# Performance work log

Hardware: AMD Instinct MI355X
Metric: run time of the kernel (lower is better)

## Reference

```python
import jax, jax.numpy as jnp
import numpy as np

# Fixed hierarchical grouping of the 15 regions into 5 groups of 3 (from split_regions)
SPLIT_IDX = np.array([[0, 1, 8], [2, 4, 6], [3, 5, 7], [9, 11, 13], [10, 12, 14]])
BN_EPS = 1e-5


def _bn_relu(x, g, b):
    # BatchNorm over (batch, spatial) dims in training-stats mode, then ReLU
    mu = jnp.mean(x, axis=(0, 2, 3), keepdims=True)
    var = jnp.var(x, axis=(0, 2, 3), keepdims=True)
    xn = (x - mu) * jax.lax.rsqrt(var + BN_EPS)
    return jax.nn.relu(xn * g[None, :, None, None] + b[None, :, None, None])


def _local_agg(x, params):
    # x: [B, Cin, G, K]; pointwise conv (1x1) -> BN -> ReLU per layer, then max over K
    for W, g, b in params:
        x = jnp.einsum('oi,bigk->bogk', W, x)
        x = _bn_relu(x, g, b)
    return jnp.max(x, axis=-1)  # [B, Cout, G]


def setup_inputs() -> dict:
    key = jax.random.key(0)
    ks = jax.random.split(key, 8)
    B, G, K = 32, 15, 2048
    inp = {"local_regions": jax.random.normal(ks[0], (B, G, K, 3), jnp.float32)}
    chans = [(3, 64, 64), (67, 128, 128), (131, 256, 256)]
    ki = 1
    for li, (c0, c1, c2) in enumerate(chans):
        for wi, (co, ci) in enumerate([(c1, c0), (c2, c1)]):
            inp[f"la{li}_w{wi}"] = jax.random.normal(ks[ki], (co, ci), jnp.float32) * (1.0 / np.sqrt(ci))
            inp[f"la{li}_g{wi}"] = jnp.ones((co,), jnp.float32)
            inp[f"la{li}_b{wi}"] = jnp.zeros((co,), jnp.float32)
            ki += 1
    return inp


def reference(local_regions,
              la0_w0, la0_g0, la0_b0, la0_w1, la0_g1, la0_b1,
              la1_w0, la1_g0, la1_b0, la1_w1, la1_g1, la1_b1,
              la2_w0, la2_g0, la2_b0, la2_w1, la2_g1, la2_b1):
    la0 = [(la0_w0, la0_g0, la0_b0), (la0_w1, la0_g1, la0_b1)]
    la1 = [(la1_w0, la1_g0, la1_b0), (la1_w1, la1_g1, la1_b1)]
    la2 = [(la2_w0, la2_g0, la2_b0), (la2_w1, la2_g1, la2_b1)]
    idx = jnp.asarray(SPLIT_IDX)

    x = jnp.transpose(local_regions, (0, 3, 1, 2))  # [B, 3, 15, K]
    centroids_1 = jnp.mean(x, axis=-1)              # [B, 3, 15]
    relative_1 = x - centroids_1[..., None]
    lf1 = _local_agg(relative_1, la0)               # [B, 64, 15]
    local_features = jnp.concatenate([centroids_1, lf1], axis=1)  # [B, 67, 15]

    # level 2: regroup 15 regions into [5, 3]
    lf1_s = jnp.transpose(lf1, (0, 2, 1))[:, idx, :]         # [B, 5, 3, 64]
    lr2 = jnp.transpose(centroids_1, (0, 2, 1))[:, idx, :]   # [B, 5, 3, 3]
    c2 = jnp.mean(lr2, axis=2)                               # [B, 5, 3]
    rel2 = lr2 - c2[:, :, None, :]
    feats2 = jnp.concatenate([rel2, lf1_s], axis=-1)         # [B, 5, 3, 67]
    feats2 = jnp.transpose(feats2, (0, 3, 1, 2))             # [B, 67, 5, 3]
    lf2 = _local_agg(feats2, la1)                            # [B, 128, 5]

    # level 3: global
    c3 = jnp.mean(c2, axis=1)                                # [B, 3]
    rel3 = c2 - c3[:, None, :]                               # [B, 5, 3]
    lf2 = jnp.concatenate([jnp.transpose(rel3, (0, 2, 1)), lf2], axis=1)  # [B, 131, 5]
    lf2 = lf2[:, :, None, :]                                 # [B, 131, 1, 5]
    gf = _local_agg(lf2, la2)                                # [B, 256, 1]
    return gf.squeeze(2), local_features
```

## Files before the change

### kernel.cpp

```cpp
#include <hip/hip_runtime.h>
#include <math.h>

#define BB 32
#define GG 15
#define KK 2048
#define NB 480
#define N1F 983040.0f
#define EPS 1e-5f
#define PZN ((int)0xAAAAAAAA)

typedef _Float16 half8 __attribute__((ext_vector_type(8)));
typedef float f32x4 __attribute__((ext_vector_type(4)));

#define WS_CENT  0
#define WS_MN    1920
#define GSREL    63360
#define GBN1     63600
#define G2A      67440
#define G2B      67952
#define G3A      68464
#define G3B      69488
#define FSREL    70512
#define FBN1     70520
#define F2A      70648
#define F2B      70904
#define F3A      71160
#define F3B      71672
#define CNT_GRP  72184
#define CNT_SUP  72376
#define CNT_DONE 72382

#define SMEMF 7936

__device__ const int SIDX[15] = {0,1,8, 2,4,6, 3,5,7, 9,11,13, 10,12,14};

__device__ __forceinline__ float wave_sum(float v){
    for (int off = 32; off; off >>= 1) v += __shfl_down(v, off, 64);
    return v;
}
__device__ __forceinline__ float aloadf(const float* p){
    return __hip_atomic_load(p, __ATOMIC_RELAXED, __HIP_MEMORY_SCOPE_AGENT);
}
__device__ __forceinline__ int aloadi(const int* p){
    return __hip_atomic_load(p, __ATOMIC_RELAXED, __HIP_MEMORY_SCOPE_AGENT);
}
template<int SLP, class Fold>
__device__ __forceinline__ void gbar(int* wsi, int idx, int gi, int ngrp,
                                     int* sflag, Fold fold){
    __syncthreads();
    if (threadIdx.x == 0)
        sflag[0] = (atomicAdd(&wsi[CNT_GRP + idx*32 + gi], 1) == PZN + 15) ? 1 : 0;
    __syncthreads();
    if (sflag[0]) {
        if (threadIdx.x == 0)
            sflag[1] = (atomicAdd(&wsi[CNT_SUP + idx], 1) == PZN + ngrp - 1) ? 1 : 0;
        __syncthreads();
        if (sflag[1]) {
            fold();
            __syncthreads();
            if (threadIdx.x == 0) atomicExch(&wsi[CNT_DONE + idx], 1);
        }
    }
    if (threadIdx.x == 0) {
        int g = 0;
        while (aloadi(&wsi[CNT_DONE + idx]) != 1 && ++g < 4000000)
            __builtin_amdgcn_s_sleep(SLP);
    }
    __syncthreads();
    asm volatile("" ::: "memory");
}

__global__ void __launch_bounds__(256, 2) mega(
        const float* __restrict__ x,
        const float* __restrict__ w00, const float* __restrict__ g00, const float* __restrict__ b00,
        const float* __restrict__ w01, const float* __restrict__ g01, const float* __restrict__ b01,
        const float* __restrict__ w10, const float* __restrict__ g10, const float* __restrict__ b10,
        const float* __restrict__ w11, const float* __restrict__ g11, const float* __restrict__ b11,
        const float* __restrict__ w20, const float* __restrict__ g20, const float* __restrict__ b20,
        const float* __restrict__ w21, const float* __restrict__ g21, const float* __restrict__ b21,
        float* __restrict__ ws, float* __restrict__ out) {
    __shared__ __align__(16) float smemf[SMEMF];
    float* xls  = smemf;
    float* redM = smemf + 6144; float* redN = smemf + 6400;
    float* redS = smemf + 6656; float* redQ = smemf + 6912;
    float* bcast= smemf + 7168;
    int*   sflag= (int*)(smemf + 7916);
    float* s1ls  = smemf;
    float* t1ls  = smemf + 64;
    float* centls= smemf + 128;
    float* c2ls  = smemf + 176;
    float* c3ls  = smemf + 192;
    float* f2ls  = smemf + 256;
    float* vls   = smemf + 1280;
    float* f3ls  = smemf + 3200;
    float* u3ls  = smemf + 3968;
    int* wsi = (int*)ws;

    int bid = blockIdx.x, tid = threadIdx.x;
    int b_ = bid / GG, g_ = bid % GG;
    int wv = tid >> 6, lane = tid & 63, l15 = lane & 15, quad = lane >> 4;
    int gi = bid >> 4;

    {
        const float4* xp4 = (const float4*)(x + (size_t)bid * KK * 3);
        float4* xls4 = (float4*)xls;
        #pragma unroll
        for (int i = 0; i < 6; i++) xls4[i*256 + tid] = xp4[i*256 + tid];
        __syncthreads();
        float m[9] = {0,0,0,0,0,0,0,0,0};
        float a[24];
        const float* bp = &xls[tid*24];
        #pragma unroll
        for (int i = 0; i < 6; i++)
            *reinterpret_cast<float4*>(&a[i*4]) = *reinterpret_cast<const float4*>(&bp[i*4]);
        #pragma unroll
        for (int p = 0; p < 8; p++) {
            float ax=a[p*3], ay=a[p*3+1], az=a[p*3+2];
            m[0]+=ax; m[1]+=ay; m[2]+=az;
            m[3]=fmaf(ax,ax,m[3]); m[4]=fmaf(ay,ay,m[4]); m[5]=fmaf(az,az,m[5]);
            m[6]=fmaf(ax,ay,m[6]); m[7]=fmaf(ax,az,m[7]); m[8]=fmaf(ay,az,m[8]);
        }
        #pragma unroll
        for (int q = 0; q < 9; q++) {
            float v = wave_sum(m[q]);
            if (lane == 0) redM[q*4 + wv] = v;
        }
        __syncthreads();
        if (tid == 0) {
            float t[9];
            #pragma unroll
            for (int q = 0; q < 9; q++) t[q] = redM[q*4]+redM[q*4+1]+redM[q*4+2]+redM[q*4+3];
            float c0 = t[0]/KK, c1 = t[1]/KK, c2 = t[2]/KK;
            bcast[0]=c0; bcast[1]=c1; bcast[2]=c2;
            out[8192 + b_*(67*GG) + 0*GG + g_] = c0;
            out[8192 + b_*(67*GG) + 1*GG + g_] = c1;
            out[8192 + b_*(67*GG) + 2*GG + g_] = c2;
            atomicExch(&ws[WS_CENT + bid*4 + 0], c0);
            atomicExch(&ws[WS_CENT + bid*4 + 1], c1);
            atomicExch(&ws[WS_CENT + bid*4 + 2], c2);
            redM[40] = t[3] - KK*c0*c0;  redM[41] = t[4] - KK*c1*c1;
            redM[42] = t[5] - KK*c2*c2;  redM[43] = t[6] - KK*c0*c1;
            redM[44] = t[7] - KK*c0*c2;  redM[45] = t[8] - KK*c1*c2;
        }
        __syncthreads();
    }
    if (tid < 6) atomicAdd(&ws[GSREL + gi*8 + tid], redM[40 + tid]);

    half8 afA[4], afB[4];
    #pragma unroll
    for (int t = 0; t < 4; t++)
        #pragma unroll
        for (int j = 0; j < 8; j++) {
            afA[t][j] = (_Float16)w01[(t*16 + l15)*64 + quad*8 + j];
            afB[t][j] = (_Float16)w01[(t*16 + l15)*64 + 32 + quad*8 + j];
        }
    gbar<8>(wsi, 0, gi, 30, sflag, [&]{
        if (tid < 6) {
            float acc = 0.f;
            #pragma unroll
            for (int s = 0; s < 30; s++) acc += aloadf(&ws[GSREL + s*8 + tid]);
            atomicExch(&ws[FSREL + tid], acc);
        }
    });

    if (tid < 6) bcast[3+tid] = aloadf(&ws[FSREL + tid]) / N1F;
    __syncthreads();
    float c0 = bcast[0], c1 = bcast[1], c2v = bcast[2];
    float S00=bcast[3], S11=bcast[4], S22=bcast[5], S01=bcast[6], S02=bcast[7], S12=bcast[8];

    float wa0[8], wa1[8], wa2[8], ba[8], wb0[8], wb1[8], wb2[8], bb[8];
    #pragma unroll
    for (int j = 0; j < 8; j++) {
        int cA = quad*8 + j;
        float u0=w00[cA*3+0], u1=w00[cA*3+1], u2=w00[cA*3+2];
        float var = u0*u0*S00 + u1*u1*S11 + u2*u2*S22
                  + 2.f*(u0*u1*S01 + u0*u2*S02 + u1*u2*S12);
        float a1 = g00[cA]*rsqrtf(var + EPS);
        wa0[j]=a1*u0; wa1[j]=a1*u1; wa2[j]=a1*u2; ba[j]=b00[cA];
        int cB = cA + 32;
        float v0=w00[cB*3+0], v1=w00[cB*3+1], v2=w00[cB*3+2];
        float varB = v0*v0*S00 + v1*v1*S11 + v2*v2*S22
                   + 2.f*(v0*v1*S01 + v0*v2*S02 + v1*v2*S12);
        float a1B = g00[cB]*rsqrtf(varB + EPS);
        wb0[j]=a1B*v0; wb1[j]=a1B*v1; wb2[j]=a1B*v2; bb[j]=b00[cB];
    }
    float mx[16], mn[16], sm[16], sq[16];
    #pragma unroll
    for (int s = 0; s < 16; s++) { mx[s]=-1e30f; mn[s]=1e30f; sm[s]=0.f; sq[s]=0.f; }

    for (int it = 0; it < 32; it++) {
        int k = it*64 + wv*16 + l15;
        float r0 = xls[k*3+0]-c0, r1 = xls[k*3+1]-c1, r2 = xls[k*3+2]-c2v;
        half8 bf0, bf1;
        #pragma unroll
        for (int j = 0; j < 8; j++) {
            float pA = fmaf(wa0[j],r0, fmaf(wa1[j],r1, fmaf(wa2[j],r2, ba[j])));
            bf0[j] = (_Float16)fmaxf(pA, 0.f);
            float pB = fmaf(wb0[j],r0, fmaf(wb1[j],r1, fmaf(wb2[j],r2, bb[j])));
            bf1[j] = (_Float16)fmaxf(pB, 0.f);
        }
        #pragma unroll
        for (int t = 0; t < 4; t++) {
            f32x4 acc = {0.f,0.f,0.f,0.f};
            acc = __builtin_amdgcn_mfma_f32_16x16x32_f16(afA[t], bf0, acc, 0, 0, 0);
            acc = __builtin_amdgcn_mfma_f32_16x16x32_f16(afB[t], bf1, acc, 0, 0, 0);
            #pragma unroll
            for (int r = 0; r < 4; r++) {
                float h = acc[r];
                int s = t*4 + r;
                mx[s]=fmaxf(mx[s],h); mn[s]=fminf(mn[s],h);
                sm[s]+=h;             sq[s]=fmaf(h,h,sq[s]);
            }
        }
    }
    #pragma unroll
    for (int m = 1; m < 16; m <<= 1) {
        #pragma unroll
        for (int s = 0; s < 16; s++) {
            mx[s] = fmaxf(mx[s], __shfl_xor(mx[s], m, 64));
            mn[s] = fminf(mn[s], __shfl_xor(mn[s], m, 64));
            sm[s] += __shfl_xor(sm[s], m, 64);
            sq[s] += __shfl_xor(sq[s], m, 64);
        }
    }
    __syncthreads();
    if (l15 == 0) {
        #pragma unroll
        for (int t = 0; t < 4; t++)
            #pragma unroll
            for (int r = 0; r < 4; r++) {
                int o = t*16 + quad*4 + r;
                redM[wv*64+o]=mx[t*4+r]; redN[wv*64+o]=mn[t*4+r];
                redS[wv*64+o]=sm[t*4+r]; redQ[wv*64+o]=sq[t*4+r];
            }
    }
    __syncthreads();
    float Mreg = -1e30f, Nreg = 1e30f;
    if (tid < 64) {
        float S=0.f, Q=0.f;
        #pragma unroll
        for (int w = 0; w < 4; w++) {
            Mreg = fmaxf(Mreg, redM[w*64+tid]); Nreg = fminf(Nreg, redN[w*64+tid]);
            S += redS[w*64+tid];               Q += redQ[w*64+tid];
        }
        atomicAdd(&ws[GBN1 + gi*128 + tid], S);
        atomicAdd(&ws[GBN1 + gi*128 + 64 + tid], Q);
        atomicExch(&ws[WS_MN + bid*128 + tid], Mreg);
        atomicExch(&ws[WS_MN + bid*128 + 64 + tid], Nreg);
    }
    gbar<8>(wsi, 1, gi, 30, sflag, [&]{
        if (tid < 128) {
            float acc = 0.f;
            #pragma unroll
            for (int s = 0; s < 30; s++) acc += aloadf(&ws[GBN1 + s*128 + tid]);
            atomicExch(&ws[FBN1 + tid], acc);
        }
    });

    if (tid < 64) {
        float SM = aloadf(&ws[FBN1 + tid]);
        float SQ = aloadf(&ws[FBN1 + 64 + tid]);
        float mean = SM / N1F;
        float var  = SQ / N1F - mean*mean;
        float s1 = g01[tid]*rsqrtf(var + EPS);
        float t1 = b01[tid] - mean*s1;
        float val = fmaxf(fmaf(s1, (s1 >= 0.f) ? Mreg : Nreg, t1), 0.f);
        out[8192 + b_*(67*GG) + (3+tid)*GG + g_] = val;
        s1ls[tid] = s1; t1ls[tid] = t1;
    }
    if (g_ != 0) return;

    int git = b_ >> 4;
    if (tid < 45) centls[tid] = aloadf(&ws[WS_CENT + (b_*GG + tid/3)*4 + tid%3]);
    __syncthreads();
    if (tid < 15) {
        int s = tid/3, i = tid%3;
        c2ls[tid] = (centls[SIDX[s*3+0]*3+i] + centls[SIDX[s*3+1]*3+i]
                   + centls[SIDX[s*3+2]*3+i]) * (1.f/3.f);
    }
    __syncthreads();
    if (tid < 3)
        c3ls[tid] = (c2ls[tid]+c2ls[3+tid]+c2ls[6+tid]+c2ls[9+tid]+c2ls[12+tid]) * 0.2f;
    if (tid < 45) {
        int p = tid/3, i = tid%3;
        f2ls[p*68 + i] = centls[SIDX[p]*3+i] - c2ls[(p/3)*3 + i];
    }
    for (int u = tid; u < 960; u += 256) {
        int p = u >> 6, ch = u & 63, gsrc = SIDX[p];
        float Mv = aloadf(&ws[WS_MN + (b_*GG + gsrc)*128 + ch]);
        float Nv = aloadf(&ws[WS_MN + (b_*GG + gsrc)*128 + 64 + ch]);
        float s1 = s1ls[ch], t1 = t1ls[ch];
        f2ls[p*68 + 3 + ch] = fmaxf(fmaf(s1, (s1 >= 0.f) ? Mv : Nv, t1), 0.f);
    }
    __syncthreads();

    int half = tid >> 7, oc = tid & 127, pbase = half*8, npts = 8 - half;
    float acc[8];
    #pragma unroll
    for (int q = 0; q < 8; q++) acc[q] = 0.f;
    {
        const float* wr = w10 + oc*67;
        #pragma unroll 4
        for (int c = 0; c < 67; c++) {
            float wv_ = wr[c];
            #pragma unroll
            for (int q = 0; q < 8; q++)
                acc[q] = fmaf(wv_, f2ls[(pbase+q)*68 + c], acc[q]);
        }
        float S = 0.f, Q = 0.f;
        #pragma unroll
        for (int q = 0; q < 8; q++) if (q < npts) { S += acc[q]; Q = fmaf(acc[q],acc[q],Q); }
        redS[tid] = S; redQ[tid] = Q;
        __syncthreads();
        if (tid < 128) {
            atomicAdd(&ws[G2A + git*256 + tid],       redS[tid] + redS[tid+128]);
            atomicAdd(&ws[G2A + git*256 + 128 + tid], redQ[tid] + redQ[tid+128]);
        }
    }
    gbar<2>(wsi, 2, git, 2, sflag, [&]{
        float a = aloadf(&ws[G2A + tid]) + aloadf(&ws[G2A + 256 + tid]);
        atomicExch(&ws[F2A + tid], a);
    });

    {
        float mean = aloadf(&ws[F2A + oc]) / 480.f;
        float var  = aloadf(&ws[F2A + 128 + oc]) / 480.f - mean*mean;
        float s2 = g10[oc]*rsqrtf(var + EPS), t2 = b10[oc] - mean*s2;
        #pragma unroll
        for (int q = 0; q < 8; q++) {
            float v = fmaxf(fmaf(s2, acc[q], t2), 0.f);
            if (q < npts) vls[(pbase+q)*128 + oc] = v;
        }
    }
    __syncthreads();
    #pragma unroll
    for (int q = 0; q < 8; q++) acc[q] = 0.f;
    {
        const float* wr = w11 + oc*128;
        #pragma unroll 4
        for (int c = 0; c < 128; c++) {
            float wv_ = wr[c];
            #pragma unroll
            for (int q = 0; q < 8; q++)
                acc[q] = fmaf(wv_, vls[(pbase+q)*128 + c], acc[q]);
        }
        float S = 0.f, Q = 0.f;
        #pragma unroll
        for (int q = 0; q < 8; q++) if (q < npts) { S += acc[q]; Q = fmaf(acc[q],acc[q],Q); }
        redS[tid] = S; redQ[tid] = Q;
        __syncthreads();
        if (tid < 128) {
            atomicAdd(&ws[G2B + git*256 + tid],       redS[tid] + redS[tid+128]);
            atomicAdd(&ws[G2B + git*256 + 128 + tid], redQ[tid] + redQ[tid+128]);
        }
    }
    gbar<2>(wsi, 3, git, 2, sflag, [&]{
        float a = aloadf(&ws[G2B + tid]) + aloadf(&ws[G2B + 256 + tid]);
        atomicExch(&ws[F2B + tid], a);
    });

    {
        float mean = aloadf(&ws[F2B + oc]) / 480.f;
        float var  = aloadf(&ws[F2B + 128 + oc]) / 480.f - mean*mean;
        float s3 = g11[oc]*rsqrtf(var + EPS), t3 = b11[oc] - mean*s3;
        #pragma unroll
        for (int q = 0; q < 8; q++) {
            float v = fmaxf(fmaf(s3, acc[q], t3), 0.f);
            if (q < npts) vls[(pbase+q)*128 + oc] = v;
        }
    }
    __syncthreads();
    for (int u = tid; u < 640; u += 256) {
        int s = u >> 7, o2 = u & 127;
        float m = fmaxf(fmaxf(vls[(3*s)*128+o2], vls[(3*s+1)*128+o2]),
                        vls[(3*s+2)*128+o2]);
        f3ls[s*132 + 3 + o2] = m;
    }
    if (tid < 15) {
        int s = tid/3, i = tid%3;
        f3ls[s*132 + i] = c2ls[tid] - c3ls[i];
    }
    __syncthreads();

    float a3[5];
    #pragma unroll
    for (int s = 0; s < 5; s++) a3[s] = 0.f;
    {
        const float* wr = w20 + tid*131;
        #pragma unroll 4
        for (int c = 0; c < 131; c++) {
            float wv_ = wr[c];
            #pragma unroll
            for (int s = 0; s < 5; s++)
                a3[s] = fmaf(wv_, f3ls[s*132 + c], a3[s]);
        }
        float S = 0.f, Q = 0.f;
        #pragma unroll
        for (int s = 0; s < 5; s++) { S += a3[s]; Q = fmaf(a3[s],a3[s],Q); }
        atomicAdd(&ws[G3A + git*512 + tid], S);
        atomicAdd(&ws[G3A + git*512 + 256 + tid], Q);
    }
    gbar<2>(wsi, 4, git, 2, sflag, [&]{
        float a0 = aloadf(&ws[G3A + tid])       + aloadf(&ws[G3A + 512 + tid]);
        float a1 = aloadf(&ws[G3A + 256 + tid]) + aloadf(&ws[G3A + 512 + 256 + tid]);
        atomicExch(&ws[F3A + tid], a0);
        atomicExch(&ws[F3A + 256 + tid], a1);
    });

    {
        float mean = aloadf(&ws[F3A + tid]) / 160.f;
        float var  = aloadf(&ws[F3A + 256 + tid]) / 160.f - mean*mean;
        float s4 = g20[tid]*rsqrtf(var + EPS), t4 = b20[tid] - mean*s4;
        #pragma unroll
        for (int s = 0; s < 5; s++)
            u3ls[s*256 + tid] = fmaxf(fmaf(s4, a3[s], t4), 0.f);
    }
    __syncthreads();
    #pragma unroll
    for (int s = 0; s < 5; s++) a3[s] = 0.f;
    {
        const float* wr = w21 + tid*256;
        #pragma unroll 4
        for (int c = 0; c < 256; c++) {
            float wv_ = wr[c];
            #pragma unroll
            for (int s = 0; s < 5; s++)
                a3[s] = fmaf(wv_, u3ls[s*256 + c], a3[s]);
        }
        float S = 0.f, Q = 0.f;
        #pragma unroll
        for (int s = 0; s < 5; s++) { S += a3[s]; Q = fmaf(a3[s],a3[s],Q); }
        atomicAdd(&ws[G3B + git*512 + tid], S);
        atomicAdd(&ws[G3B + git*512 + 256 + tid], Q);
    }
    gbar<2>(wsi, 5, git, 2, sflag, [&]{
        float a0 = aloadf(&ws[G3B + tid])       + aloadf(&ws[G3B + 512 + tid]);
        float a1 = aloadf(&ws[G3B + 256 + tid]) + aloadf(&ws[G3B + 512 + 256 + tid]);
        atomicExch(&ws[F3B + tid], a0);
        atomicExch(&ws[F3B + 256 + tid], a1);
    });

    {
        float mean = aloadf(&ws[F3B + tid]) / 160.f;
        float var  = aloadf(&ws[F3B + 256 + tid]) / 160.f - mean*mean;
        float s5 = g21[tid]*rsqrtf(var + EPS), t5 = b21[tid] - mean*s5;
        float m = -1e30f;
        #pragma unroll
        for (int s = 0; s < 5; s++)
            m = fmaxf(m, fmaxf(fmaf(s5, a3[s], t5), 0.f));
        out[b_*256 + tid] = m;
    }
}

extern "C" void kernel_launch(void* const* d_in, const int* in_sizes, int n_in,
                              void* d_out, int out_size, void* d_ws, size_t ws_size,
                              hipStream_t stream) {
    (void)in_sizes; (void)n_in; (void)out_size; (void)ws_size;
    const float* x   = (const float*)d_in[0];
    const float* w00 = (const float*)d_in[1];
    const float* g00 = (const float*)d_in[2];
    const float* b00 = (const float*)d_in[3];
    const float* w01 = (const float*)d_in[4];
    const float* g01 = (const float*)d_in[5];
    const float* b01 = (const float*)d_in[6];
    const float* w10 = (const float*)d_in[7];
    const float* g10 = (const float*)d_in[8];
    const float* b10 = (const float*)d_in[9];
    const float* w11 = (const float*)d_in[10];
    const float* g11 = (const float*)d_in[11];
    const float* b11 = (const float*)d_in[12];
    const float* w20 = (const float*)d_in[13];
    const float* g20 = (const float*)d_in[14];
    const float* b20 = (const float*)d_in[15];
    const float* w21 = (const float*)d_in[16];
    const float* g21 = (const float*)d_in[17];
    const float* b21 = (const float*)d_in[18];
    float* out = (float*)d_out;
    float* ws  = (float*)d_ws;

    mega<<<NB, 256, 0, stream>>>(x, w00,g00,b00, w01,g01,b01, w10,g10,b10,
                                 w11,g11,b11, w20,g20,b20, w21,g21,b21, ws, out);
}
```

Before: 191.1 us.

## Compute level-2/3 BN statistics in one block with MFMA, publish coefficients via flags

Instead of per-batch blocks exchanging partial BN sums through grid-wide atomic barriers at each later layer, block 0 recomputes all 480 level-2 points (and level-3) in fp16 MFMA to derive the BN scale/shift coefficients. It publishes them to workspace and sets done flags. Other blocks do their fp32 matmuls and only wait on those flags before applying normalization. It also stores only the sign-selected max/min per channel, halving that workspace traffic. This removes several multi-block barrier rounds, but serializes a large redundant computation on block 0 and uses fp16 for the statistics.

```diff
diff --git a/kernel.cpp b/kernel.cpp
--- a/kernel.cpp
+++ b/kernel.cpp
@@ -13,24 +13,22 @@
 typedef float f32x4 __attribute__((ext_vector_type(4)));
 
 #define WS_CENT  0
-#define WS_MN    1920
-#define GSREL    63360
-#define GBN1     63600
-#define G2A      67440
-#define G2B      67952
-#define G3A      68464
-#define G3B      69488
-#define FSREL    70512
-#define FBN1     70520
-#define F2A      70648
-#define F2B      70904
-#define F3A      71160
-#define F3B      71672
-#define CNT_GRP  72184
-#define CNT_SUP  72376
-#define CNT_DONE 72382
-
-#define SMEMF 7936
+#define WS_SEL   1920
+#define GSREL    32640
+#define GBN1     32880
+#define FSREL    36720
+#define FBN1     36728
+#define COEF2    36856
+#define COEF3    37112
+#define COEF4    37368
+#define COEF5    37880
+#define SCR1     38392
+#define SCR2     53752
+#define CNT_GRP  58872
+#define CNT_SUP  58936
+#define CNT_DONE 58942
+
+#define SMEMF 8832
 
 __device__ const int SIDX[15] = {0,1,8, 2,4,6, 3,5,7, 9,11,13, 10,12,14};
 
@@ -69,6 +67,18 @@
     __syncthreads();
     asm volatile("" ::: "memory");
 }
+__device__ __forceinline__ void waitflag(int* wsi, int idx){
+    __syncthreads();
+    if (threadIdx.x == 0) {
+        int g = 0;
+        while (aloadi(&wsi[CNT_DONE + idx]) != 1 && ++g < 4000000)
+            __builtin_amdgcn_s_sleep(2);
+    }
+    __syncthreads();
+    asm volatile("" ::: "memory");
+}
+
+union HPK { _Float16 h[2]; unsigned int w; };
 
 __global__ void __launch_bounds__(256, 2) mega(
         const float* __restrict__ x,
@@ -87,13 +97,6 @@
     int*   sflag= (int*)(smemf + 7916);
     float* s1ls  = smemf;
     float* t1ls  = smemf + 64;
-    float* centls= smemf + 128;
-    float* c2ls  = smemf + 176;
-    float* c3ls  = smemf + 192;
-    float* f2ls  = smemf + 256;
-    float* vls   = smemf + 1280;
-    float* f3ls  = smemf + 3200;
-    float* u3ls  = smemf + 3968;
     int* wsi = (int*)ws;
 
     int bid = blockIdx.x, tid = threadIdx.x;
@@ -245,8 +248,8 @@
         }
         atomicAdd(&ws[GBN1 + gi*128 + tid], S);
         atomicAdd(&ws[GBN1 + gi*128 + 64 + tid], Q);
-        atomicExch(&ws[WS_MN + bid*128 + tid], Mreg);
-        atomicExch(&ws[WS_MN + bid*128 + 64 + tid], Nreg);
+        float sel = (g01[tid] >= 0.f) ? Mreg : Nreg;
+        atomicExch(&ws[WS_SEL + bid*64 + tid], sel);
     }
     gbar<8>(wsi, 1, gi, 30, sflag, [&]{
         if (tid < 128) {
@@ -268,187 +271,596 @@
         out[8192 + b_*(67*GG) + (3+tid)*GG + g_] = val;
         s1ls[tid] = s1; t1ls[tid] = t1;
     }
-    if (g_ != 0) return;
-
-    int git = b_ >> 4;
-    if (tid < 45) centls[tid] = aloadf(&ws[WS_CENT + (b_*GG + tid/3)*4 + tid%3]);
-    __syncthreads();
-    if (tid < 15) {
-        int s = tid/3, i = tid%3;
-        c2ls[tid] = (centls[SIDX[s*3+0]*3+i] + centls[SIDX[s*3+1]*3+i]
-                   + centls[SIDX[s*3+2]*3+i]) * (1.f/3.f);
-    }
-    __syncthreads();
-    if (tid < 3)
-        c3ls[tid] = (c2ls[tid]+c2ls[3+tid]+c2ls[6+tid]+c2ls[9+tid]+c2ls[12+tid]) * 0.2f;
-    if (tid < 45) {
-        int p = tid/3, i = tid%3;
-        f2ls[p*68 + i] = centls[SIDX[p]*3+i] - c2ls[(p/3)*3 + i];
-    }
-    for (int u = tid; u < 960; u += 256) {
-        int p = u >> 6, ch = u & 63, gsrc = SIDX[p];
-        float Mv = aloadf(&ws[WS_MN + (b_*GG + gsrc)*128 + ch]);
-        float Nv = aloadf(&ws[WS_MN + (b_*GG + gsrc)*128 + 64 + ch]);
-        float s1 = s1ls[ch], t1 = t1ls[ch];
-        f2ls[p*68 + 3 + ch] = fmaxf(fmaf(s1, (s1 >= 0.f) ? Mv : Nv, t1), 0.f);
-    }
-    __syncthreads();
-
-    int half = tid >> 7, oc = tid & 127, pbase = half*8, npts = 8 - half;
-    float acc[8];
-    #pragma unroll
-    for (int q = 0; q < 8; q++) acc[q] = 0.f;
+
+    if (bid == 0) {
+        float* statS = smemf + 128;
+        float* statQ = smemf + 384;
+        float* s2ls = smemf + 640;  float* t2ls = smemf + 768;
+        float* s3ls = smemf + 896;  float* t3ls = smemf + 1024;
+        float* s4ls = smemf + 1152; float* t4ls = smemf + 1408;
+        float* w10c = smemf + 1664;
+        float* w20c = smemf + 2176;
+        _Float16* rel2f = (_Float16*)(smemf + 3200);
+        _Float16* rel3f = (_Float16*)(smemf + 4160);
+        float* centa = smemf + 4736;
+        float* c2a   = smemf + 6176;
+        float* c3a   = smemf + 6656;
+        _Float16* vtb = (_Float16*)(smemf + 4608);
+        unsigned int* scru1 = (unsigned int*)(ws + SCR1);
+        unsigned int* scru2 = (unsigned int*)(ws + SCR2);
+
+        for (int u = tid; u < 1440; u += 256)
+            centa[u] = aloadf(&ws[WS_CENT + (u/3)*4 + u%3]);
+        for (int u = tid; u < 384; u += 256)
+            w10c[(u/3)*4 + u%3] = w10[(u/3)*67 + u%3];
+        for (int u = tid; u < 768; u += 256)
+            w20c[(u/3)*4 + u%3] = w20[(u/3)*131 + u%3];
+        __syncthreads();
+        for (int u = tid; u < 480; u += 256) {
+            int b = u/15, r = u%15, s = r/3, i = r%3;
+            c2a[u] = (centa[(b*15+SIDX[s*3+0])*3+i] + centa[(b*15+SIDX[s*3+1])*3+i]
+                    + centa[(b*15+SIDX[s*3+2])*3+i]) * (1.f/3.f);
+        }
+        __syncthreads();
+        for (int u = tid; u < 96; u += 256) {
+            int b = u/3, i = u%3;
+            c3a[u] = (c2a[(b*5+0)*3+i]+c2a[(b*5+1)*3+i]+c2a[(b*5+2)*3+i]
+                     +c2a[(b*5+3)*3+i]+c2a[(b*5+4)*3+i])*0.2f;
+        }
+        __syncthreads();
+        for (int u = tid; u < 1440; u += 256) {
+            int n = u/3, i = u%3, b = n/15, p = n%15;
+            rel2f[n*4+i] = (_Float16)(centa[(b*15+SIDX[p])*3+i] - c2a[(b*5+p/3)*3+i]);
+        }
+        for (int u = tid; u < 480; u += 256) {
+            int sp = u/3, i = u%3;
+            rel3f[sp*4+i] = (_Float16)(c2a[sp*3+i] - c3a[(sp/5)*3+i]);
+        }
+        for (int u = tid; u < 15360; u += 256) {
+            int n = u>>5, cp = u&31, ch = cp*2;
+            int b = n/15, p = n%15, src = b*15 + SIDX[p];
+            float se0 = aloadf(&ws[WS_SEL + src*64 + ch]);
+            float se1 = aloadf(&ws[WS_SEL + src*64 + ch + 1]);
+            HPK pk;
+            pk.h[0] = (_Float16)fmaxf(fmaf(s1ls[ch],   se0, t1ls[ch]),   0.f);
+            pk.h[1] = (_Float16)fmaxf(fmaf(s1ls[ch+1], se1, t1ls[ch+1]), 0.f);
+            scru1[u] = pk.w;
+        }
+        __syncthreads();
+
+        half8 a10[2][2], a11[2][4];
+        #pragma unroll
+        for (int mt2 = 0; mt2 < 2; mt2++) {
+            #pragma unroll
+            for (int kt = 0; kt < 2; kt++)
+                #pragma unroll
+                for (int j = 0; j < 8; j++)
+                    a10[mt2][kt][j] = (_Float16)w10[((2*wv+mt2)*16 + l15)*67 + 3 + kt*32 + quad*8 + j];
+            #pragma unroll
+            for (int kt = 0; kt < 4; kt++)
+                #pragma unroll
+                for (int j = 0; j < 8; j++)
+                    a11[mt2][kt][j] = (_Float16)w11[((2*wv+mt2)*16 + l15)*128 + kt*32 + quad*8 + j];
+        }
+
+        {
+            float sS[2][4], sQ[2][4];
+            #pragma unroll
+            for (int m2 = 0; m2 < 2; m2++)
+                #pragma unroll
+                for (int r = 0; r < 4; r++) { sS[m2][r]=0.f; sQ[m2][r]=0.f; }
+            for (int nt = 0; nt < 30; nt++) {
+                int n = nt*16 + l15;
+                half8 bf[2];
+                #pragma unroll
+                for (int kt = 0; kt < 2; kt++)
+                    bf[kt] = *(const half8*)(scru1 + n*32 + kt*16 + quad*4);
+                #pragma unroll
+                for (int m2 = 0; m2 < 2; m2++) {
+                    f32x4 acc;
+                    #pragma unroll
+                    for (int r = 0; r < 4; r++) {
+                        int row = (2*wv+m2)*16 + quad*4 + r;
+                        acc[r] = w10c[row*4+0]*(float)rel2f[n*4+0]
+                               + w10c[row*4+1]*(float)rel2f[n*4+1]
+                               + w10c[row*4+2]*(float)rel2f[n*4+2];
+                    }
+                    acc = __builtin_amdgcn_mfma_f32_16x16x32_f16(a10[m2][0], bf[0], acc, 0,0,0);
+                    acc = __builtin_amdgcn_mfma_f32_16x16x32_f16(a10[m2][1], bf[1], acc, 0,0,0);
+                    #pragma unroll
+                    for (int r = 0; r < 4; r++) {
+                        sS[m2][r] += acc[r]; sQ[m2][r] = fmaf(acc[r],acc[r],sQ[m2][r]);
+                    }
+                }
+            }
+            #pragma unroll
+            for (int m = 1; m < 16; m <<= 1)
+                #pragma unroll
+                for (int m2 = 0; m2 < 2; m2++)
+                    #pragma unroll
+                    for (int r = 0; r < 4; r++) {
+                        sS[m2][r] += __shfl_xor(sS[m2][r], m, 64);
+                        sQ[m2][r] += __shfl_xor(sQ[m2][r], m, 64);
+                    }
+            if (l15 == 0) {
+                #pragma unroll
+                for (int m2 = 0; m2 < 2; m2++)
+                    #pragma unroll
+                    for (int r = 0; r < 4; r++) {
+                        int row = (2*wv+m2)*16 + quad*4 + r;
+                        statS[row] = sS[m2][r]; statQ[row] = sQ[m2][r];
+                    }
+            }
+            __syncthreads();
+            if (tid < 128) {
+                float mean = statS[tid]/480.f, var = statQ[tid]/480.f - mean*mean;
+                float s2 = g10[tid]*rsqrtf(var+EPS), t2 = b10[tid] - mean*s2;
+                s2ls[tid]=s2; t2ls[tid]=t2;
+                atomicExch(&ws[COEF2+tid], s2); atomicExch(&ws[COEF2+128+tid], t2);
+            }
+            __syncthreads();
+            if (tid == 0) atomicExch(&wsi[CNT_DONE + 2], 1);
+        }
+
+        {
+            float sS[2][4], sQ[2][4];
+            #pragma unroll
+            for (int m2 = 0; m2 < 2; m2++)
+                #pragma unroll
+                for (int r = 0; r < 4; r++) { sS[m2][r]=0.f; sQ[m2][r]=0.f; }
+            for (int c = 0; c < 10; c++) {
+                #pragma unroll
+                for (int ntl = 0; ntl < 3; ntl++) {
+                    int n = (c*3 + ntl)*16 + l15;
+                    half8 bf[2];
+                    #pragma unroll
+                    for (int kt = 0; kt < 2; kt++)
+                        bf[kt] = *(const half8*)(scru1 + n*32 + kt*16 + quad*4);
+                    #pragma unroll
+                    for (int m2 = 0; m2 < 2; m2++) {
+                        f32x4 acc;
+                        #pragma unroll
+                        for (int r = 0; r < 4; r++) {
+                            int row = (2*wv+m2)*16 + quad*4 + r;
+                            acc[r] = w10c[row*4+0]*(float)rel2f[n*4+0]
+                                   + w10c[row*4+1]*(float)rel2f[n*4+1]
+                                   + w10c[row*4+2]*(float)rel2f[n*4+2];
+                        }
+                        acc = __builtin_amdgcn_mfma_f32_16x16x32_f16(a10[m2][0], bf[0], acc, 0,0,0);
+                        acc = __builtin_amdgcn_mfma_f32_16x16x32_f16(a10[m2][1], bf[1], acc, 0,0,0);
+                        #pragma unroll
+                        for (int rp = 0; rp < 2; rp++) {
+                            int row0 = (2*wv+m2)*16 + quad*4 + rp*2;
+                            HPK pk;
+                            pk.h[0] = (_Float16)fmaxf(fmaf(s2ls[row0],   acc[rp*2],   t2ls[row0]),   0.f);
+                            pk.h[1] = (_Float16)fmaxf(fmaf(s2ls[row0+1], acc[rp*2+1], t2ls[row0+1]), 0.f);
+                            *(unsigned int*)&vtb[(ntl*16+l15)*136 + row0] = pk.w;
+                        }
+                    }
+                }
+                __syncthreads();
+                #pragma unroll
+                for (int ntl = 0; ntl < 3; ntl++) {
+                    half8 bv[4];
+                    #pragma unroll
+                    for (int kt = 0; kt < 4; kt++)
+                        bv[kt] = *(const half8*)&vtb[(ntl*16+l15)*136 + kt*32 + quad*8];
+                    #pragma unroll
+                    for (int m2 = 0; m2 < 2; m2++) {
+                        f32x4 acc = {0.f,0.f,0.f,0.f};
+                        #pragma unroll
+                        for (int kt = 0; kt < 4; kt++)
+                            acc = __builtin_amdgcn_mfma_f32_16x16x32_f16(a11[m2][kt], bv[kt], acc, 0,0,0);
+                        #pragma unroll
+                        for (int r = 0; r < 4; r++) {
+                            sS[m2][r] += acc[r]; sQ[m2][r] = fmaf(acc[r],acc[r],sQ[m2][r]);
+                        }
+                    }
+                }
+                __syncthreads();
+            }
+            #pragma unroll
+            for (int m = 1; m < 16; m <<= 1)
+                #pragma unroll
+                for (int m2 = 0; m2 < 2; m2++)
+                    #pragma unroll
+                    for (int r = 0; r < 4; r++) {
+                        sS[m2][r] += __shfl_xor(sS[m2][r], m, 64);
+                        sQ[m2][r] += __shfl_xor(sQ[m2][r], m, 64);
+                    }
+            if (l15 == 0) {
+                #pragma unroll
+                for (int m2 = 0; m2 < 2; m2++)
+                    #pragma unroll
+                    for (int r = 0; r < 4; r++) {
+                        int row = (2*wv+m2)*16 + quad*4 + r;
+                        statS[row] = sS[m2][r]; statQ[row] = sQ[m2][r];
+                    }
+            }
+            __syncthreads();
+            if (tid < 128) {
+                float mean = statS[tid]/480.f, var = statQ[tid]/480.f - mean*mean;
+                float s3 = g11[tid]*rsqrtf(var+EPS), t3 = b11[tid] - mean*s3;
+                s3ls[tid]=s3; t3ls[tid]=t3;
+                atomicExch(&ws[COEF3+tid], s3); atomicExch(&ws[COEF3+128+tid], t3);
+            }
+            __syncthreads();
+            if (tid == 0) atomicExch(&wsi[CNT_DONE + 3], 1);
+        }
+
+        for (int c = 0; c < 10; c++) {
+            #pragma unroll
+            for (int ntl = 0; ntl < 3; ntl++) {
+                int n = (c*3 + ntl)*16 + l15;
+                half8 bf[2];
+                #pragma unroll
+                for (int kt = 0; kt < 2; kt++)
+                    bf[kt] = *(const half8*)(scru1 + n*32 + kt*16 + quad*4);
+                #pragma unroll
+                for (int m2 = 0; m2 < 2; m2++) {
+                    f32x4 acc;
+                    #pragma unroll
+                    for (int r = 0; r < 4; r++) {
+                        int row = (2*wv+m2)*16 + quad*4 + r;
+                        acc[r] = w10c[row*4+0]*(float)rel2f[n*4+0]
+                               + w10c[row*4+1]*(float)rel2f[n*4+1]
+                               + w10c[row*4+2]*(float)rel2f[n*4+2];
+                    }
+                    acc = __builtin_amdgcn_mfma_f32_16x16x32_f16(a10[m2][0], bf[0], acc, 0,0,0);
+                    acc = __builtin_amdgcn_mfma_f32_16x16x32_f16(a10[m2][1], bf[1], acc, 0,0,0);
+                    #pragma unroll
+                    for (int rp = 0; rp < 2; rp++) {
+                        int row0 = (2*wv+m2)*16 + quad*4 + rp*2;
+                        HPK pk;
+                        pk.h[0] = (_Float16)fmaxf(fmaf(s2ls[row0],   acc[rp*2],   t2ls[row0]),   0.f);
+                        pk.h[1] = (_Float16)fmaxf(fmaf(s2ls[row0+1], acc[rp*2+1], t2ls[row0+1]), 0.f);
+                        *(unsigned int*)&vtb[(ntl*16+l15)*136 + row0] = pk.w;
+                    }
+                }
+            }
+            __syncthreads();
+            f32x4 h2b[3][2];
+            #pragma unroll
+            for (int ntl = 0; ntl < 3; ntl++) {
+                half8 bv[4];
+                #pragma unroll
+                for (int kt = 0; kt < 4; kt++)
+                    bv[kt] = *(const half8*)&vtb[(ntl*16+l15)*136 + kt*32 + quad*8];
+                #pragma unroll
+                for (int m2 = 0; m2 < 2; m2++) {
+                    f32x4 acc = {0.f,0.f,0.f,0.f};
+                    #pragma unroll
+                    for (int kt = 0; kt < 4; kt++)
+                        acc = __builtin_amdgcn_mfma_f32_16x16x32_f16(a11[m2][kt], bv[kt], acc, 0,0,0);
+                    h2b[ntl][m2] = acc;
+                }
+            }
+            __syncthreads();
+            #pragma unroll
+            for (int ntl = 0; ntl < 3; ntl++)
+                #pragma unroll
+                for (int m2 = 0; m2 < 2; m2++)
+                    #pragma unroll
+                    for (int rp = 0; rp < 2; rp++) {
+                        int row0 = (2*wv+m2)*16 + quad*4 + rp*2;
+                        HPK pk;
+                        pk.h[0] = (_Float16)fmaxf(fmaf(s3ls[row0],   h2b[ntl][m2][rp*2],   t3ls[row0]),   0.f);
+                        pk.h[1] = (_Float16)fmaxf(fmaf(s3ls[row0+1], h2b[ntl][m2][rp*2+1], t3ls[row0+1]), 0.f);
+                        *(unsigned int*)&vtb[(ntl*16+l15)*136 + row0] = pk.w;
+                    }
+            __syncthreads();
+            for (int u = tid; u < 1024; u += 256) {
+                int sl = u >> 6, cp = u & 63, ch = cp*2;
+                float m0 = fmaxf(fmaxf((float)vtb[(3*sl+0)*136+ch],   (float)vtb[(3*sl+1)*136+ch]),
+                                 (float)vtb[(3*sl+2)*136+ch]);
+                float m1 = fmaxf(fmaxf((float)vtb[(3*sl+0)*136+ch+1], (float)vtb[(3*sl+1)*136+ch+1]),
+                                 (float)vtb[(3*sl+2)*136+ch+1]);
+                HPK pk; pk.h[0] = (_Float16)m0; pk.h[1] = (_Float16)m1;
+                scru2[(c*16+sl)*64 + cp] = pk.w;
+            }
+            __syncthreads();
+        }
+
+        {
+            float sS[4][4], sQ[4][4];
+            #pragma unroll
+            for (int ml = 0; ml < 4; ml++)
+                #pragma unroll
+                for (int r = 0; r < 4; r++) { sS[ml][r]=0.f; sQ[ml][r]=0.f; }
+            #pragma unroll
+            for (int ml = 0; ml < 4; ml++) {
+                int mt = wv*4 + ml;
+                half8 a20[4];
+                #pragma unroll
+                for (int kt = 0; kt < 4; kt++)
+                    #pragma unroll
+                    for (int j = 0; j < 8; j++)
+                        a20[kt][j] = (_Float16)w20[(mt*16+l15)*131 + 3 + kt*32 + quad*8 + j];
+                for (int nt = 0; nt < 10; nt++) {
+                    int sp = nt*16 + l15;
+                    half8 bl[4];
+                    #pragma unroll
+                    for (int kt = 0; kt < 4; kt++)
+                        bl[kt] = *(const half8*)(scru2 + sp*64 + kt*16 + quad*4);
+                    f32x4 acc;
+                    #pragma unroll
+                    for (int r = 0; r < 4; r++) {
+                        int row = mt*16 + quad*4 + r;
+                        acc[r] = w20c[row*4+0]*(float)rel3f[sp*4+0]
+                               + w20c[row*4+1]*(float)rel3f[sp*4+1]
+                               + w20c[row*4+2]*(float)rel3f[sp*4+2];
+                    }
+                    #pragma unroll
+                    for (int kt = 0; kt < 4; kt++)
+                        acc = __builtin_amdgcn_mfma_f32_16x16x32_f16(a20[kt], bl[kt], acc, 0,0,0);
+                    #pragma unroll
+                    for (int r = 0; r < 4; r++) {
+                        sS[ml][r] += acc[r]; sQ[ml][r] = fmaf(acc[r],acc[r],sQ[ml][r]);
+                    }
+                }
+            }
+            #pragma unroll
+            for (int m = 1; m < 16; m <<= 1)
+                #pragma unroll
+                for (int ml = 0; ml < 4; ml++)
+                    #pragma unroll
+                    for (int r = 0; r < 4; r++) {
+                        sS[ml][r] += __shfl_xor(sS[ml][r], m, 64);
+                        sQ[ml][r] += __shfl_xor(sQ[ml][r], m, 64);
+                    }
+            if (l15 == 0) {
+                #pragma unroll
+                for (int ml = 0; ml < 4; ml++)
+                    #pragma unroll
+                    for (int r = 0; r < 4; r++) {
+                        int row = (wv*4+ml)*16 + quad*4 + r;
+                        statS[row] = sS[ml][r]; statQ[row] = sQ[ml][r];
+                    }
+            }
+            __syncthreads();
+            {
+                float mean = statS[tid]/160.f, var = statQ[tid]/160.f - mean*mean;
+                float s4 = g20[tid]*rsqrtf(var+EPS), t4 = b20[tid] - mean*s4;
+                s4ls[tid]=s4; t4ls[tid]=t4;
+                atomicExch(&ws[COEF4+tid], s4); atomicExch(&ws[COEF4+256+tid], t4);
+            }
+            __syncthreads();
+            if (tid == 0) atomicExch(&wsi[CNT_DONE + 4], 1);
+        }
+
+        {
+            float sS[4][4], sQ[4][4];
+            #pragma unroll
+            for (int ml = 0; ml < 4; ml++)
+                #pragma unroll
+                for (int r = 0; r < 4; r++) { sS[ml][r]=0.f; sQ[ml][r]=0.f; }
+            for (int cc = 0; cc < 5; cc++) {
+                #pragma unroll
+                for (int ml = 0; ml < 4; ml++) {
+                    int mt = wv*4 + ml;
+                    half8 a20[4];
+                    #pragma unroll
+                    for (int kt = 0; kt < 4; kt++)
+                        #pragma unroll
+                        for (int j = 0; j < 8; j++)
+                            a20[kt][j] = (_Float16)w20[(mt*16+l15)*131 + 3 + kt*32 + quad*8 + j];
+                    #pragma unroll
+                    for (int ntl = 0; ntl < 2; ntl++) {
+                        int sp = (cc*2+ntl)*16 + l15;
+                        half8 bl[4];
+                        #pragma unroll
+                        for (int kt = 0; kt < 4; kt++)
+                            bl[kt] = *(const half8*)(scru2 + sp*64 + kt*16 + quad*4);
+                        f32x4 acc;
+                        #pragma unroll
+                        for (int r = 0; r < 4; r++) {
+                            int row = mt*16 + quad*4 + r;
+                            acc[r] = w20c[row*4+0]*(float)rel3f[sp*4+0]
+                                   + w20c[row*4+1]*(float)rel3f[sp*4+1]
+                                   + w20c[row*4+2]*(float)rel3f[sp*4+2];
+                        }
+                        #pragma unroll
+                        for (int kt = 0; kt < 4; kt++)
+                            acc = __builtin_amdgcn_mfma_f32_16x16x32_f16(a20[kt], bl[kt], acc, 0,0,0);
+                        #pragma unroll
+                        for (int rp = 0; rp < 2; rp++) {
+                            int row0 = mt*16 + quad*4 + rp*2;
+                            HPK pk;
+                            pk.h[0] = (_Float16)fmaxf(fmaf(s4ls[row0],   acc[rp*2],   t4ls[row0]),   0.f);
+                            pk.h[1] = (_Float16)fmaxf(fmaf(s4ls[row0+1], acc[rp*2+1], t4ls[row0+1]), 0.f);
+                            *(unsigned int*)&vtb[(ntl*16+l15)*264 + row0] = pk.w;
+                        }
+                    }
+                }
+                __syncthreads();
+                #pragma unroll
+                for (int ml = 0; ml < 4; ml++) {
+                    int mt = wv*4 + ml;
+                    half8 a21[8];
+                    #pragma unroll
+                    for (int kt = 0; kt < 8; kt++)
+                        #pragma unroll
+                        for (int j = 0; j < 8; j++)
+                            a21[kt][j] = (_Float16)w21[(mt*16+l15)*256 + kt*32 + quad*8 + j];
+                    #pragma unroll
+                    for (int ntl = 0; ntl < 2; ntl++) {
+                        half8 bu[8];
+                        #pragma unroll
+                        for (int kt = 0; kt < 8; kt++)
+                            bu[kt] = *(const half8*)&vtb[(ntl*16+l15)*264 + kt*32 + quad*8];
+                        f32x4 acc = {0.f,0.f,0.f,0.f};
+                        #pragma unroll
+                        for (int kt = 0; kt < 8; kt++)
+                            acc = __builtin_amdgcn_mfma_f32_16x16x32_f16(a21[kt], bu[kt], acc, 0,0,0);
+                        #pragma unroll
+                        for (int r = 0; r < 4; r++) {
+                            sS[ml][r] += acc[r]; sQ[ml][r] = fmaf(acc[r],acc[r],sQ[ml][r]);
+                        }
+                    }
+                }
+                __syncthreads();
+            }
+            #pragma unroll
+            for (int m = 1; m < 16; m <<= 1)
+                #pragma unroll
+                for (int ml = 0; ml < 4; ml++)
+                    #pragma unroll
+                    for (int r = 0; r < 4; r++) {
+                        sS[ml][r] += __shfl_xor(sS[ml][r], m, 64);
+                        sQ[ml][r] += __shfl_xor(sQ[ml][r], m, 64);
+                    }
+            if (l15 == 0) {
+                #pragma unroll
+                for (int ml = 0; ml < 4; ml++)
+                    #pragma unroll
+                    for (int r = 0; r < 4; r++) {
+                        int row = (wv*4+ml)*16 + quad*4 + r;
+                        statS[row] = sS[ml][r]; statQ[row] = sQ[ml][r];
+                    }
+            }
+            __syncthreads();
+            {
+                float mean = statS[tid]/160.f, var = statQ[tid]/160.f - mean*mean;
+                float s5 = g21[tid]*rsqrtf(var+EPS), t5 = b21[tid] - mean*s5;
+                atomicExch(&ws[COEF5+tid], s5); atomicExch(&ws[COEF5+256+tid], t5);
+            }
+            __syncthreads();
+            if (tid == 0) atomicExch(&wsi[CNT_DONE + 5], 1);
+        }
+        return;
+    }
+    if (g_ != 1) return;
+
     {
-        const float* wr = w10 + oc*67;
-        #pragma unroll 4
-        for (int c = 0; c < 67; c++) {
-            float wv_ = wr[c];
-            #pragma unroll
-            for (int q = 0; q < 8; q++)
-                acc[q] = fmaf(wv_, f2ls[(pbase+q)*68 + c], acc[q]);
-        }
-        float S = 0.f, Q = 0.f;
-        #pragma unroll
-        for (int q = 0; q < 8; q++) if (q < npts) { S += acc[q]; Q = fmaf(acc[q],acc[q],Q); }
-        redS[tid] = S; redQ[tid] = Q;
-        __syncthreads();
-        if (tid < 128) {
-            atomicAdd(&ws[G2A + git*256 + tid],       redS[tid] + redS[tid+128]);
-            atomicAdd(&ws[G2A + git*256 + 128 + tid], redQ[tid] + redQ[tid+128]);
-        }
-    }
-    gbar<2>(wsi, 2, git, 2, sflag, [&]{
-        float a = aloadf(&ws[G2A + tid]) + aloadf(&ws[G2A + 256 + tid]);
-        atomicExch(&ws[F2A + tid], a);
-    });
-
-    {
-        float mean = aloadf(&ws[F2A + oc]) / 480.f;
-        float var  = aloadf(&ws[F2A + 128 + oc]) / 480.f - mean*mean;
-        float s2 = g10[oc]*rsqrtf(var + EPS), t2 = b10[oc] - mean*s2;
-        #pragma unroll
-        for (int q = 0; q < 8; q++) {
-            float v = fmaxf(fmaf(s2, acc[q], t2), 0.f);
-            if (q < npts) vls[(pbase+q)*128 + oc] = v;
-        }
-    }
-    __syncthreads();
-    #pragma unroll
-    for (int q = 0; q < 8; q++) acc[q] = 0.f;
-    {
-        const float* wr = w11 + oc*128;
-        #pragma unroll 4
-        for (int c = 0; c < 128; c++) {
-            float wv_ = wr[c];
-            #pragma unroll
-            for (int q = 0; q < 8; q++)
-                acc[q] = fmaf(wv_, vls[(pbase+q)*128 + c], acc[q]);
-        }
-        float S = 0.f, Q = 0.f;
-        #pragma unroll
-        for (int q = 0; q < 8; q++) if (q < npts) { S += acc[q]; Q = fmaf(acc[q],acc[q],Q); }
-        redS[tid] = S; redQ[tid] = Q;
-        __syncthreads();
-        if (tid < 128) {
-            atomicAdd(&ws[G2B + git*256 + tid],       redS[tid] + redS[tid+128]);
-            atomicAdd(&ws[G2B + git*256 + 128 + tid], redQ[tid] + redQ[tid+128]);
-        }
-    }
-    gbar<2>(wsi, 3, git, 2, sflag, [&]{
-        float a = aloadf(&ws[G2B + tid]) + aloadf(&ws[G2B + 256 + tid]);
-        atomicExch(&ws[F2B + tid], a);
-    });
-
-    {
-        float mean = aloadf(&ws[F2B + oc]) / 480.f;
-        float var  = aloadf(&ws[F2B + 128 + oc]) / 480.f - mean*mean;
-        float s3 = g11[oc]*rsqrtf(var + EPS), t3 = b11[oc] - mean*s3;
-        #pragma unroll
-        for (int q = 0; q < 8; q++) {
-            float v = fmaxf(fmaf(s3, acc[q], t3), 0.f);
-            if (q < npts) vls[(pbase+q)*128 + oc] = v;
-        }
-    }
-    __syncthreads();
-    for (int u = tid; u < 640; u += 256) {
-        int s = u >> 7, o2 = u & 127;
-        float m = fmaxf(fmaxf(vls[(3*s)*128+o2], vls[(3*s+1)*128+o2]),
-                        vls[(3*s+2)*128+o2]);
-        f3ls[s*132 + 3 + o2] = m;
-    }
-    if (tid < 15) {
-        int s = tid/3, i = tid%3;
-        f3ls[s*132 + i] = c2ls[tid] - c3ls[i];
-    }
-    __syncthreads();
-
-    float a3[5];
-    #pragma unroll
-    for (int s = 0; s < 5; s++) a3[s] = 0.f;
-    {
-        const float* wr = w20 + tid*131;
-        #pragma unroll 4
-        for (int c = 0; c < 131; c++) {
-            float wv_ = wr[c];
+        float* centb = smemf + 128;
+        float* c2b   = smemf + 176;
+        float* c3b   = smemf + 192;
+        float* f2b   = smemf + 256;
+        float* vb    = smemf + 1280;
+        float* f3b   = smemf + 3328;
+        float* u3b   = smemf + 3988;
+
+        if (tid < 45) centb[tid] = aloadf(&ws[WS_CENT + (b_*GG + tid/3)*4 + tid%3]);
+        __syncthreads();
+        if (tid < 15) {
+            int s = tid/3, i = tid%3;
+            c2b[tid] = (centb[SIDX[s*3+0]*3+i] + centb[SIDX[s*3+1]*3+i]
+                      + centb[SIDX[s*3+2]*3+i]) * (1.f/3.f);
+        }
+        __syncthreads();
+        if (tid < 3)
+            c3b[tid] = (c2b[tid]+c2b[3+tid]+c2b[6+tid]+c2b[9+tid]+c2b[12+tid]) * 0.2f;
+        if (tid < 45) {
+            int p = tid/3, i = tid%3;
+            f2b[p*68 + i] = centb[SIDX[p]*3+i] - c2b[(p/3)*3 + i];
+        }
+        for (int u = tid; u < 960; u += 256) {
+            int p = u >> 6, ch = u & 63, src = b_*GG + SIDX[p];
+            float sel = aloadf(&ws[WS_SEL + src*64 + ch]);
+            f2b[p*68 + 3 + ch] = fmaxf(fmaf(s1ls[ch], sel, t1ls[ch]), 0.f);
+        }
+        __syncthreads();
+
+        int half = tid >> 7, oc = tid & 127, pbase = half*8, npts = 8 - half;
+        float acc[8];
+        #pragma unroll
+        for (int q = 0; q < 8; q++) acc[q] = 0.f;
+        {
+            const float* wr = w10 + oc*67;
+            #pragma unroll 4
+            for (int c = 0; c < 67; c++) {
+                float wv_ = wr[c];
+                #pragma unroll
+                for (int q = 0; q < 8; q++)
+                    acc[q] = fmaf(wv_, f2b[(pbase+q)*68 + c], acc[q]);
+            }
+        }
+        waitflag(wsi, 2);
+        {
+            float s2 = aloadf(&ws[COEF2 + oc]), t2 = aloadf(&ws[COEF2 + 128 + oc]);
+            #pragma unroll
+            for (int q = 0; q < 8; q++) {
+                float v = fmaxf(fmaf(s2, acc[q], t2), 0.f);
+                if (q < npts) vb[(pbase+q)*128 + oc] = v;
+            }
+        }
+        __syncthreads();
+        float acc2[8];
+        #pragma unroll
+        for (int q = 0; q < 8; q++) acc2[q] = 0.f;
+        {
+            const float* wr = w11 + oc*128;
+            #pragma unroll 4
+            for (int c = 0; c < 128; c++) {
+                float wv_ = wr[c];
+                #pragma unroll
+                for (int q = 0; q < 8; q++)
+                    acc2[q] = fmaf(wv_, vb[(pbase+q)*128 + c], acc2[q]);
+            }
+        }
+        waitflag(wsi, 3);
+        {
+            float s3 = aloadf(&ws[COEF3 + oc]), t3 = aloadf(&ws[COEF3 + 128 + oc]);
+            #pragma unroll
+            for (int q = 0; q < 8; q++) {
+                float v = fmaxf(fmaf(s3, acc2[q], t3), 0.f);
+                if (q < npts) vb[(pbase+q)*128 + oc] = v;
+            }
+        }
+        __syncthreads();
+        for (int u = tid; u < 640; u += 256) {
+            int s = u >> 7, ch = u & 127;
+            f3b[s*132 + 3 + ch] = fmaxf(fmaxf(vb[(3*s)*128+ch], vb[(3*s+1)*128+ch]),
+                                        vb[(3*s+2)*128+ch]);
+        }
+        if (tid < 15) {
+            int s = tid/3, i = tid%3;
+            f3b[s*132 + i] = c2b[tid] - c3b[i];
+        }
+        __syncthreads();
+        float a3[5];
+        #pragma unroll
+        for (int s = 0; s < 5; s++) a3[s] = 0.f;
+        {
+            const float* wr = w20 + tid*131;
+            #pragma unroll 4
+            for (int c = 0; c < 131; c++) {
+                float wv_ = wr[c];
+                #pragma unroll
+                for (int s = 0; s < 5; s++)
+                    a3[s] = fmaf(wv_, f3b[s*132 + c], a3[s]);
+            }
+        }
+        waitflag(wsi, 4);
+        {
+            float s4 = aloadf(&ws[COEF4 + tid]), t4 = aloadf(&ws[COEF4 + 256 + tid]);
             #pragma unroll
             for (int s = 0; s < 5; s++)
-                a3[s] = fmaf(wv_, f3ls[s*132 + c], a3[s]);
-        }
-        float S = 0.f, Q = 0.f;
-        #pragma unroll
-        for (int s = 0; s < 5; s++) { S += a3[s]; Q = fmaf(a3[s],a3[s],Q); }
-        atomicAdd(&ws[G3A + git*512 + tid], S);
-        atomicAdd(&ws[G3A + git*512 + 256 + tid], Q);
-    }
-    gbar<2>(wsi, 4, git, 2, sflag, [&]{
-        float a0 = aloadf(&ws[G3A + tid])       + aloadf(&ws[G3A + 512 + tid]);
-        float a1 = aloadf(&ws[G3A + 256 + tid]) + aloadf(&ws[G3A + 512 + 256 + tid]);
-        atomicExch(&ws[F3A + tid], a0);
-        atomicExch(&ws[F3A + 256 + tid], a1);
-    });
-
-    {
-        float mean = aloadf(&ws[F3A + tid]) / 160.f;
-        float var  = aloadf(&ws[F3A + 256 + tid]) / 160.f - mean*mean;
-        float s4 = g20[tid]*rsqrtf(var + EPS), t4 = b20[tid] - mean*s4;
-        #pragma unroll
-        for (int s = 0; s < 5; s++)
-            u3ls[s*256 + tid] = fmaxf(fmaf(s4, a3[s], t4), 0.f);
-    }
-    __syncthreads();
-    #pragma unroll
-    for (int s = 0; s < 5; s++) a3[s] = 0.f;
-    {
-        const float* wr = w21 + tid*256;
-        #pragma unroll 4
-        for (int c = 0; c < 256; c++) {
-            float wv_ = wr[c];
+                u3b[s*256 + tid] = fmaxf(fmaf(s4, a3[s], t4), 0.f);
+        }
+        __syncthreads();
+        float a3b[5];
+        #pragma unroll
+        for (int s = 0; s < 5; s++) a3b[s] = 0.f;
+        {
+            const float* wr = w21 + tid*256;
+            #pragma unroll 4
+            for (int c = 0; c < 256; c++) {
+                float wv_ = wr[c];
+                #pragma unroll
+                for (int s = 0; s < 5; s++)
+                    a3b[s] = fmaf(wv_, u3b[s*256 + c], a3b[s]);
+            }
+        }
+        waitflag(wsi, 5);
+        {
+            float s5 = aloadf(&ws[COEF5 + tid]), t5 = aloadf(&ws[COEF5 + 256 + tid]);
+            float m = -1e30f;
             #pragma unroll
             for (int s = 0; s < 5; s++)
-                a3[s] = fmaf(wv_, u3ls[s*256 + c], a3[s]);
-        }
-        float S = 0.f, Q = 0.f;
-        #pragma unroll
-        for (int s = 0; s < 5; s++) { S += a3[s]; Q = fmaf(a3[s],a3[s],Q); }
-        atomicAdd(&ws[G3B + git*512 + tid], S);
-        atomicAdd(&ws[G3B + git*512 + 256 + tid], Q);
-    }
-    gbar<2>(wsi, 5, git, 2, sflag, [&]{
-        float a0 = aloadf(&ws[G3B + tid])       + aloadf(&ws[G3B + 512 + tid]);
-        float a1 = aloadf(&ws[G3B + 256 + tid]) + aloadf(&ws[G3B + 512 + 256 + tid]);
-        atomicExch(&ws[F3B + tid], a0);
-        atomicExch(&ws[F3B + 256 + tid], a1);
-    });
-
-    {
-        float mean = aloadf(&ws[F3B + tid]) / 160.f;
-        float var  = aloadf(&ws[F3B + 256 + tid]) / 160.f - mean*mean;
-        float s5 = g21[tid]*rsqrtf(var + EPS), t5 = b21[tid] - mean*s5;
-        float m = -1e30f;
-        #pragma unroll
-        for (int s = 0; s < 5; s++)
-            m = fmaxf(m, fmaxf(fmaf(s5, a3[s], t5), 0.f));
-        out[b_*256 + tid] = m;
+                m = fmaxf(m, fmaxf(fmaf(s5, a3b[s], t5), 0.f));
+            out[b_*256 + tid] = m;
+        }
     }
 }
 
```

Result: slower. 310.0 us (+62.2%).
